# Kernel optimization log

Measured on AMD Instinct MI355X. Metric: run time of the kernel, lower is better.

The kernel has to match this reference:

```python
import jax, jax.numpy as jnp
import numpy as np

B, S, D = 2, 2048, 2048
H, HD = 16, 128
F = 8192
LC = 512
EPS = 1e-6


def _linear_params(k, din, dout):
    k1, k2 = jax.random.split(k)
    w = jax.random.normal(k1, (din, dout), jnp.float32) * 0.02
    b = jax.random.normal(k2, (dout,), jnp.float32) * 0.02
    return w, b


def setup_inputs() -> dict:
    key = jax.random.key(0)
    ks = jax.random.split(key, 20)
    inp = {}
    inp["x"] = jax.random.normal(ks[0], (B, S, D), jnp.float32)
    inp["e"] = jax.random.normal(ks[1], (B, 6, D), jnp.float32) * 0.1
    inp["context"] = jax.random.normal(ks[2], (B, LC, D), jnp.float32)
    # per-token rotary angles [S, HD//2] (Wan builds such a table from 3D grid)
    inp["freqs"] = jax.random.uniform(ks[3], (S, HD // 2), jnp.float32) * (2.0 * np.pi)
    inp["modulation"] = jax.random.normal(ks[4], (1, 6, D), jnp.float32) / np.sqrt(D)
    names = ["sq", "sk", "sv", "so", "cq", "ck", "cv", "co"]
    for i, nm in enumerate(names):
        w, b = _linear_params(ks[5 + i], D, D)
        inp[nm + "_w"], inp[nm + "_b"] = w, b
    inp["f1_w"], inp["f1_b"] = _linear_params(ks[13], D, F)
    inp["f2_w"], inp["f2_b"] = _linear_params(ks[14], F, D)
    inp["snq"] = jnp.ones((D,), jnp.float32)
    inp["snk"] = jnp.ones((D,), jnp.float32)
    inp["cnq"] = jnp.ones((D,), jnp.float32)
    inp["cnk"] = jnp.ones((D,), jnp.float32)
    return inp


def _rmsnorm(x, w):
    # WanRMSNorm: x * rsqrt(mean(x^2) + eps) * weight
    return x * jax.lax.rsqrt(jnp.mean(x * x, axis=-1, keepdims=True) + EPS) * w


def _layernorm(x):
    # elementwise_affine=False LayerNorm
    m = jnp.mean(x, axis=-1, keepdims=True)
    v = jnp.mean((x - m) ** 2, axis=-1, keepdims=True)
    return (x - m) * jax.lax.rsqrt(v + EPS)


def _rope(x, ang):
    # x: [B, S, H, HD]; ang: [S, HD//2]; adjacent pairs rotated (view_as_complex)
    c = jnp.cos(ang)[None, :, None, :]
    s = jnp.sin(ang)[None, :, None, :]
    xr, xi = x[..., 0::2], x[..., 1::2]
    out = jnp.stack([xr * c - xi * s, xr * s + xi * c], axis=-1)
    return out.reshape(x.shape)


def _attn(q, k, v):
    # q: [B,Sq,H,HD], k/v: [B,Sk,H,HD] -> [B,Sq,H,HD]
    scores = jnp.einsum("bqhd,bkhd->bhqk", q, k) / np.sqrt(HD)
    probs = jax.nn.softmax(scores, axis=-1)
    return jnp.einsum("bhqk,bkhd->bqhd", probs, v)


def reference(x, e, context, freqs, modulation,
              sq_w, sq_b, sk_w, sk_b, sv_w, sv_b, so_w, so_b, snq, snk,
              cq_w, cq_b, ck_w, ck_b, cv_w, cv_b, co_w, co_b, cnq, cnk,
              f1_w, f1_b, f2_w, f2_b):
    em = modulation + e  # [B,6,D]
    e0, e1, e2, e3, e4, e5 = [em[:, i:i + 1, :] for i in range(6)]

    # self-attention with AdaLN modulation
    tx = _layernorm(x) * (1.0 + e1) + e0
    q = _rmsnorm(tx @ sq_w + sq_b, snq).reshape(B, S, H, HD)
    k = _rmsnorm(tx @ sk_w + sk_b, snk).reshape(B, S, H, HD)
    v = (tx @ sv_w + sv_b).reshape(B, S, H, HD)
    q, k = _rope(q, freqs), _rope(k, freqs)
    y = _attn(q, k, v).reshape(B, S, D) @ so_w + so_b
    x = x + y * e2

    # cross-attention (norm3 = Identity since cross_attn_norm=False)
    q = _rmsnorm(x @ cq_w + cq_b, cnq).reshape(B, S, H, HD)
    k = _rmsnorm(context @ ck_w + ck_b, cnk).reshape(B, LC, H, HD)
    v = (context @ cv_w + cv_b).reshape(B, LC, H, HD)
    x = x + (_attn(q, k, v).reshape(B, S, D) @ co_w + co_b)

    # FFN with AdaLN modulation
    tx = _layernorm(x) * (1.0 + e4) + e3
    y = jax.nn.gelu(tx @ f1_w + f1_b, approximate=True) @ f2_w + f2_b
    x = x + y * e5
    return x
```

## Files before the change

### kernel.cpp

```cpp
#include <hip/hip_runtime.h>
#include <hip/hip_bf16.h>

using bf16 = __hip_bfloat16;
typedef __attribute__((ext_vector_type(8))) short bf16x8;
typedef __attribute__((ext_vector_type(4))) float f32x4;
typedef const __attribute__((address_space(1))) unsigned int* gp_t;
typedef __attribute__((address_space(3))) unsigned int* sp_t;

#define B_   2
#define S_   2048
#define D_   2048
#define H_   16
#define HD_  128
#define F_   8192
#define LC_  512
#define ESTRIDE (6*D_)

__device__ __forceinline__ float bsum4(float v, float* rs) {
  #pragma unroll
  for (int o = 32; o; o >>= 1) v += __shfl_down(v, o, 64);
  int lane = threadIdx.x & 63, w = threadIdx.x >> 6;
  if (!lane) rs[w] = v;
  __syncthreads();
  float r = rs[0] + rs[1] + rs[2] + rs[3];
  __syncthreads();
  return r;
}
__device__ __forceinline__ float bmax4(float v, float* rs) {
  #pragma unroll
  for (int o = 32; o; o >>= 1) v = fmaxf(v, __shfl_down(v, o, 64));
  int lane = threadIdx.x & 63, w = threadIdx.x >> 6;
  if (!lane) rs[w] = v;
  __syncthreads();
  float r = fmaxf(fmaxf(rs[0], rs[1]), fmaxf(rs[2], rs[3]));
  __syncthreads();
  return r;
}

__global__ void k_addmod(const float* __restrict__ e, const float* __restrict__ mod,
                         float* __restrict__ em) {
  int i = blockIdx.x * 256 + threadIdx.x;
  em[i] = e[i] + mod[i % (6 * D_)];
}

__global__ void k_f2b(const float* __restrict__ in, bf16* __restrict__ out) {
  int i = blockIdx.x * 256 + threadIdx.x;
  out[i] = __float2bfloat16(in[i]);
}

__global__ void k_copy_f32(const float* __restrict__ in, float* __restrict__ out) {
  int i = blockIdx.x * 256 + threadIdx.x;
  out[i] = in[i];
}

__global__ void k_tr_f2b(const float* __restrict__ in, bf16* __restrict__ out,
                         int K, int N) {
  __shared__ float tile[64][65];
  int kb = blockIdx.y << 6, nb = blockIdx.x << 6;
  int x = threadIdx.x & 63, y = threadIdx.x >> 6;
  #pragma unroll
  for (int r = y; r < 64; r += 4) tile[r][x] = in[(size_t)(kb + r) * N + nb + x];
  __syncthreads();
  #pragma unroll
  for (int r = y; r < 64; r += 4)
    out[(size_t)(nb + r) * K + kb + x] = __float2bfloat16(tile[x][r]);
}

__global__ void k_tr_b2b(const bf16* __restrict__ in, bf16* __restrict__ out,
                         int R, int C, long long sIn, long long sOut) {
  in  += (long long)blockIdx.z * sIn;
  out += (long long)blockIdx.z * sOut;
  __shared__ bf16 tile[64][65];
  int rb = blockIdx.y << 6, cb = blockIdx.x << 6;
  int x = threadIdx.x & 63, y = threadIdx.x >> 6;
  #pragma unroll
  for (int r = y; r < 64; r += 4) tile[r][x] = in[(size_t)(rb + r) * C + cb + x];
  __syncthreads();
  #pragma unroll
  for (int r = y; r < 64; r += 4) out[(size_t)(cb + r) * R + rb + x] = tile[x][r];
}

__global__ void k_ln_mod(const float* __restrict__ x, const float* __restrict__ em,
                         int i0, int i1, bf16* __restrict__ out, int s_per_b) {
  __shared__ float rs[4];
  int row = blockIdx.x, t = threadIdx.x;
  int b = row / s_per_b;
  const float* xr = x + (size_t)row * D_;
  float vals[8], s = 0.f, ss = 0.f;
  #pragma unroll
  for (int j = 0; j < 8; j++) {
    float v = xr[t + j * 256];
    vals[j] = v; s += v; ss += v * v;
  }
  s  = bsum4(s, rs);
  ss = bsum4(ss, rs);
  float mean = s * (1.f / D_);
  float var  = ss * (1.f / D_) - mean * mean;
  float inv  = rsqrtf(var + 1e-6f);
  const float* e0 = em + ((size_t)b * 6 + i0) * D_;
  const float* e1 = em + ((size_t)b * 6 + i1) * D_;
  bf16* orow = out + (size_t)row * D_;
  #pragma unroll
  for (int j = 0; j < 8; j++) {
    int c = t + j * 256;
    orow[c] = __float2bfloat16((vals[j] - mean) * inv * (1.f + e1[c]) + e0[c]);
  }
}

__global__ void k_rms_rope(bf16* __restrict__ buf, const float* __restrict__ w,
                           const float* __restrict__ freqs, int do_rope, int s_per_b) {
  __shared__ float rs[4];
  int row = blockIdx.x, t = threadIdx.x;
  bf16* pr = buf + (size_t)row * D_;
  float4 raw = *(const float4*)(pr + (size_t)t * 8);
  bf16* hb = (bf16*)&raw;
  float v[8], ss = 0.f;
  #pragma unroll
  for (int j = 0; j < 8; j++) { v[j] = __bfloat162float(hb[j]); ss += v[j] * v[j]; }
  ss = bsum4(ss, rs);
  float inv = rsqrtf(ss * (1.f / D_) + 1e-6f);
  int base = t * 8;
  #pragma unroll
  for (int j = 0; j < 8; j++) v[j] = v[j] * inv * w[base + j];
  if (do_rope) {
    int s = row % s_per_b;
    const float* fr = freqs + (size_t)s * (HD_ / 2) + ((base & (HD_ - 1)) >> 1);
    #pragma unroll
    for (int p = 0; p < 4; p++) {
      float ang = fr[p];
      float c = cosf(ang), sn = sinf(ang);
      float xr = v[2 * p], xi = v[2 * p + 1];
      v[2 * p]     = xr * c - xi * sn;
      v[2 * p + 1] = xr * sn + xi * c;
    }
  }
  float4 ow; bf16* ho = (bf16*)&ow;
  #pragma unroll
  for (int j = 0; j < 8; j++) ho[j] = __float2bfloat16(v[j]);
  *(float4*)(pr + (size_t)t * 8) = ow;
}

template <int EPT>
__global__ void k_softmax(bf16* __restrict__ buf, int N) {
  __shared__ float rs[4];
  int row = blockIdx.x, t = threadIdx.x;
  bf16* pr = buf + (size_t)row * N;
  float v[EPT], mx = -1e30f;
  #pragma unroll
  for (int j = 0; j < EPT; j++) { v[j] = __bfloat162float(pr[t + j * 256]); mx = fmaxf(mx, v[j]); }
  mx = bmax4(mx, rs);
  float s = 0.f;
  #pragma unroll
  for (int j = 0; j < EPT; j++) { v[j] = __expf(v[j] - mx); s += v[j]; }
  s = bsum4(s, rs);
  float invs = 1.f / s;
  #pragma unroll
  for (int j = 0; j < EPT; j++) pr[t + j * 256] = __float2bfloat16(v[j] * invs);
}

__device__ __forceinline__ void xcd_swizzle(int& bx, int& by) {
  int nx = gridDim.x, ny = gridDim.y;
  if ((nx & 7) == 0) {
    int flat = by * nx + bx;
    int xcd = flat & 7;
    int idx = flat >> 3;
    int sx = nx >> 3;
    bx = xcd * sx + (idx % sx);
    by = idx / sx;
    (void)ny;
  }
}

template <int EPI>
__global__ __launch_bounds__(256) void gemm_bt(
    const bf16* __restrict__ A, int lda, long long sA,
    const bf16* __restrict__ Bt, int ldb, long long sB,
    const float* __restrict__ bias,
    bf16* __restrict__ Cb, int ldc, long long sCb,
    float* __restrict__ Cf, const float* __restrict__ Xin,
    float scale, const float* __restrict__ evec, int s_per_b,
    int K) {
  __shared__ __align__(16) bf16 As[128][32];
  __shared__ __align__(16) bf16 Bs[128][32];
  const int z = blockIdx.z;
  A  += (long long)z * sA;
  Bt += (long long)z * sB;
  int bx = blockIdx.x, by = blockIdx.y;
  xcd_swizzle(bx, by);
  const int m0 = by * 128, n0 = bx * 128;
  const int t = threadIdx.x;
  const int w = t >> 6, lane = t & 63;
  const int wrow = (w >> 1) * 64, wcol = (w & 1) * 64;
  const int quad = lane >> 4, l16 = lane & 15;

  f32x4 zero = {0.f, 0.f, 0.f, 0.f};
  f32x4 acc[4][4];
  #pragma unroll
  for (int i = 0; i < 4; i++)
    #pragma unroll
    for (int j = 0; j < 4; j++) acc[i][j] = zero;

  for (int k0 = 0; k0 < K; k0 += 32) {
    #pragma unroll
    for (int i = 0; i < 2; i++) {
      int c = t + i * 256;
      int r = c >> 2, col = (c & 3) * 8;
      __builtin_amdgcn_global_load_lds(
          (gp_t)(A + (size_t)(m0 + r) * lda + k0 + col),
          (sp_t)(&As[0][0] + (size_t)(w * 64 + i * 256) * 8), 16, 0, 0);
      __builtin_amdgcn_global_load_lds(
          (gp_t)(Bt + (size_t)(n0 + r) * ldb + k0 + col),
          (sp_t)(&Bs[0][0] + (size_t)(w * 64 + i * 256) * 8), 16, 0, 0);
    }
    __syncthreads();
    bf16x8 af[4], bfr[4];
    #pragma unroll
    for (int mi = 0; mi < 4; mi++) af[mi]  = *(const bf16x8*)(&As[wrow + mi * 16 + l16][quad * 8]);
    #pragma unroll
    for (int ni = 0; ni < 4; ni++) bfr[ni] = *(const bf16x8*)(&Bs[wcol + ni * 16 + l16][quad * 8]);
    #pragma unroll
    for (int mi = 0; mi < 4; mi++)
      #pragma unroll
      for (int ni = 0; ni < 4; ni++)
        acc[mi][ni] = __builtin_amdgcn_mfma_f32_16x16x32_bf16(af[mi], bfr[ni], acc[mi][ni], 0, 0, 0);
    __syncthreads();
  }

  #pragma unroll
  for (int mi = 0; mi < 4; mi++) {
    #pragma unroll
    for (int r = 0; r < 4; r++) {
      int gm = m0 + wrow + mi * 16 + quad * 4 + r;
      #pragma unroll
      for (int ni = 0; ni < 4; ni++) {
        int gn = n0 + wcol + ni * 16 + l16;
        float v = acc[mi][ni][r];
        if (EPI == 0) {
          if (bias) v += bias[gn];
          Cb[(long long)z * sCb + (size_t)gm * ldc + gn] = __float2bfloat16(v);
        } else if (EPI == 1) {
          Cb[(long long)z * sCb + (size_t)gm * ldc + gn] = __float2bfloat16(v * scale);
        } else if (EPI == 3) {
          v += bias[gn];
          float g = 0.5f * v * (1.f + tanhf(0.7978845608028654f * (v + 0.044715f * v * v * v)));
          Cb[(long long)z * sCb + (size_t)gm * ldc + gn] = __float2bfloat16(g);
        } else {
          v += bias[gn];
          if (evec) v *= evec[(size_t)(gm / s_per_b) * ESTRIDE + gn];
          float o = Xin[(size_t)gm * ldc + gn] + v;
          Cf[(size_t)gm * ldc + gn] = o;
          if (Cb) Cb[(size_t)gm * ldc + gn] = __float2bfloat16(o);
        }
      }
    }
  }
}

__global__ __launch_bounds__(256) void gemm64(
    const bf16* __restrict__ A, int lda, long long sA,
    const bf16* __restrict__ Bt, int ldb, long long sB,
    bf16* __restrict__ Cb, int ldc, long long sCb,
    int K) {
  __shared__ __align__(16) bf16 As[64][32];
  __shared__ __align__(16) bf16 Bs[64][32];
  const int z = blockIdx.z;
  A  += (long long)z * sA;
  Bt += (long long)z * sB;
  const int m0 = blockIdx.y * 64, n0 = blockIdx.x * 64;
  const int t = threadIdx.x;
  const int w = t >> 6, lane = t & 63;
  const int wrow = (w >> 1) * 32, wcol = (w & 1) * 32;
  const int quad = lane >> 4, l16 = lane & 15;

  f32x4 zero = {0.f, 0.f, 0.f, 0.f};
  f32x4 acc[2][2];
  #pragma unroll
  for (int i = 0; i < 2; i++)
    #pragma unroll
    for (int j = 0; j < 2; j++) acc[i][j] = zero;

  for (int k0 = 0; k0 < K; k0 += 32) {
    {
      int r = t >> 2, col = (t & 3) * 8;
      __builtin_amdgcn_global_load_lds(
          (gp_t)(A + (size_t)(m0 + r) * lda + k0 + col),
          (sp_t)(&As[0][0] + (size_t)(w * 64) * 8), 16, 0, 0);
      __builtin_amdgcn_global_load_lds(
          (gp_t)(Bt + (size_t)(n0 + r) * ldb + k0 + col),
          (sp_t)(&Bs[0][0] + (size_t)(w * 64) * 8), 16, 0, 0);
    }
    __syncthreads();
    bf16x8 af[2], bfr[2];
    #pragma unroll
    for (int mi = 0; mi < 2; mi++) af[mi]  = *(const bf16x8*)(&As[wrow + mi * 16 + l16][quad * 8]);
    #pragma unroll
    for (int ni = 0; ni < 2; ni++) bfr[ni] = *(const bf16x8*)(&Bs[wcol + ni * 16 + l16][quad * 8]);
    #pragma unroll
    for (int mi = 0; mi < 2; mi++)
      #pragma unroll
      for (int ni = 0; ni < 2; ni++)
        acc[mi][ni] = __builtin_amdgcn_mfma_f32_16x16x32_bf16(af[mi], bfr[ni], acc[mi][ni], 0, 0, 0);
    __syncthreads();
  }

  #pragma unroll
  for (int mi = 0; mi < 2; mi++) {
    #pragma unroll
    for (int r = 0; r < 4; r++) {
      int gm = m0 + wrow + mi * 16 + quad * 4 + r;
      #pragma unroll
      for (int ni = 0; ni < 2; ni++) {
        int gn = n0 + wcol + ni * 16 + l16;
        Cb[(long long)z * sCb + (size_t)gm * ldc + gn] = __float2bfloat16(acc[mi][ni][r]);
      }
    }
  }
}

extern "C" void kernel_launch(void* const* d_in, const int* in_sizes, int n_in,
                              void* d_out, int out_size, void* d_ws, size_t ws_size,
                              hipStream_t stream) {
  const float* x     = (const float*)d_in[0];
  const float* e     = (const float*)d_in[1];
  const float* ctx   = (const float*)d_in[2];
  const float* freqs = (const float*)d_in[3];
  const float* modu  = (const float*)d_in[4];
  const float* sq_w = (const float*)d_in[5];  const float* sq_b = (const float*)d_in[6];
  const float* sk_w = (const float*)d_in[7];  const float* sk_b = (const float*)d_in[8];
  const float* sv_w = (const float*)d_in[9];  const float* sv_b = (const float*)d_in[10];
  const float* so_w = (const float*)d_in[11]; const float* so_b = (const float*)d_in[12];
  const float* cq_w = (const float*)d_in[13]; const float* cq_b = (const float*)d_in[14];
  const float* ck_w = (const float*)d_in[15]; const float* ck_b = (const float*)d_in[16];
  const float* cv_w = (const float*)d_in[17]; const float* cv_b = (const float*)d_in[18];
  const float* co_w = (const float*)d_in[19]; const float* co_b = (const float*)d_in[20];
  const float* f1_w = (const float*)d_in[21]; const float* f1_b = (const float*)d_in[22];
  const float* f2_w = (const float*)d_in[23]; const float* f2_b = (const float*)d_in[24];
  const float* snq  = (const float*)d_in[25]; const float* snk  = (const float*)d_in[26];
  const float* cnq  = (const float*)d_in[27]; const float* cnk  = (const float*)d_in[28];
  float* out = (float*)d_out;

  const size_t MD = (size_t)B_ * S_ * D_;

  char* W = (char*)d_ws;
  size_t off = 0;
  auto alloc = [&](size_t bytes) -> char* {
    char* p = W + off; off += (bytes + 255) & ~(size_t)255; return p;
  };
  float* em  = (float*)alloc((size_t)B_ * 6 * D_ * 4);
  bf16* wT   = (bf16*)alloc((size_t)F_ * D_ * 2);
  bf16* vb   = (bf16*)alloc(MD * 2);
  bf16* tx   = (bf16*)alloc(MD * 2);
  bf16* qb   = (bf16*)alloc(MD * 2);
  bf16* kb   = (bf16*)alloc(MD * 2);
  bf16* vt   = (bf16*)alloc(MD * 2);
  bf16* attnout = (bf16*)alloc(MD * 2);
  bf16* ctxb = (bf16*)alloc((size_t)B_ * LC_ * D_ * 2);
  bf16* kc   = (bf16*)alloc((size_t)B_ * LC_ * D_ * 2);
  bf16* vc   = (bf16*)alloc((size_t)B_ * LC_ * D_ * 2);
  bf16* vtc  = (bf16*)alloc((size_t)B_ * LC_ * D_ * 2);
  bf16* scores8 = wT;
  bf16* scoresC = wT;
  bf16* mid = qb;
  if (off > ws_size) {
    k_copy_f32<<<(int)(MD / 256), 256, 0, stream>>>(x, out);
    return;
  }

  const float qk_scale = 0.08838834764831845f;

  k_addmod<<<(B_ * 6 * D_) / 256, 256, 0, stream>>>(e, modu, em);
  k_f2b<<<(B_ * LC_ * D_) / 256, 256, 0, stream>>>(ctx, ctxb);

  k_ln_mod<<<B_ * S_, 256, 0, stream>>>(x, em, 0, 1, tx, S_);
  k_tr_f2b<<<dim3(D_ / 64, D_ / 64), 256, 0, stream>>>(sq_w, wT, D_, D_);
  gemm_bt<0><<<dim3(16, 32, 1), 256, 0, stream>>>(tx, D_, 0, wT, D_, 0, sq_b,
      qb, D_, 0, nullptr, nullptr, 1.f, nullptr, S_, D_);
  k_tr_f2b<<<dim3(D_ / 64, D_ / 64), 256, 0, stream>>>(sk_w, wT, D_, D_);
  gemm_bt<0><<<dim3(16, 32, 1), 256, 0, stream>>>(tx, D_, 0, wT, D_, 0, sk_b,
      kb, D_, 0, nullptr, nullptr, 1.f, nullptr, S_, D_);
  k_tr_f2b<<<dim3(D_ / 64, D_ / 64), 256, 0, stream>>>(sv_w, wT, D_, D_);
  gemm_bt<0><<<dim3(16, 32, 1), 256, 0, stream>>>(tx, D_, 0, wT, D_, 0, sv_b,
      vb, D_, 0, nullptr, nullptr, 1.f, nullptr, S_, D_);
  k_rms_rope<<<B_ * S_, 256, 0, stream>>>(qb, snq, freqs, 1, S_);
  k_rms_rope<<<B_ * S_, 256, 0, stream>>>(kb, snk, freqs, 1, S_);
  k_tr_b2b<<<dim3(D_ / 64, S_ / 64, B_), 256, 0, stream>>>(vb, vt, S_, D_,
      (long long)S_ * D_, (long long)D_ * S_);

  for (int b = 0; b < B_; b++) {
    for (int hc = 0; hc < 2; hc++) {
      const int h0 = hc * 8;
      const bf16* Aq = qb + (size_t)b * S_ * D_ + h0 * HD_;
      const bf16* Bk = kb + (size_t)b * S_ * D_ + h0 * HD_;
      gemm_bt<1><<<dim3(16, 16, 8), 256, 0, stream>>>(Aq, D_, HD_, Bk, D_, HD_, nullptr,
          scores8, S_, (long long)S_ * S_, nullptr, nullptr, qk_scale, nullptr, S_, HD_);
      k_softmax<8><<<8 * S_, 256, 0, stream>>>(scores8, S_);
      const bf16* Bv = vt + ((size_t)b * D_ + h0 * HD_) * S_;
      gemm64<<<dim3(2, 32, 8), 256, 0, stream>>>(scores8, S_, (long long)S_ * S_,
          Bv, S_, (long long)HD_ * S_,
          attnout + (size_t)b * S_ * D_ + h0 * HD_, D_, HD_, S_);
    }
  }
  k_tr_f2b<<<dim3(D_ / 64, D_ / 64), 256, 0, stream>>>(so_w, wT, D_, D_);
  gemm_bt<2><<<dim3(16, 32, 1), 256, 0, stream>>>(attnout, D_, 0, wT, D_, 0, so_b,
      tx, D_, 0, out, x, 1.f, em + 2 * D_, S_, D_);

  k_tr_f2b<<<dim3(D_ / 64, D_ / 64), 256, 0, stream>>>(cq_w, wT, D_, D_);
  gemm_bt<0><<<dim3(16, 32, 1), 256, 0, stream>>>(tx, D_, 0, wT, D_, 0, cq_b,
      qb, D_, 0, nullptr, nullptr, 1.f, nullptr, S_, D_);
  k_rms_rope<<<B_ * S_, 256, 0, stream>>>(qb, cnq, nullptr, 0, S_);
  k_tr_f2b<<<dim3(D_ / 64, D_ / 64), 256, 0, stream>>>(ck_w, wT, D_, D_);
  gemm_bt<0><<<dim3(16, 8, 1), 256, 0, stream>>>(ctxb, D_, 0, wT, D_, 0, ck_b,
      kc, D_, 0, nullptr, nullptr, 1.f, nullptr, S_, D_);
  k_rms_rope<<<B_ * LC_, 256, 0, stream>>>(kc, cnk, nullptr, 0, S_);
  k_tr_f2b<<<dim3(D_ / 64, D_ / 64), 256, 0, stream>>>(cv_w, wT, D_, D_);
  gemm_bt<0><<<dim3(16, 8, 1), 256, 0, stream>>>(ctxb, D_, 0, wT, D_, 0, cv_b,
      vc, D_, 0, nullptr, nullptr, 1.f, nullptr, S_, D_);
  k_tr_b2b<<<dim3(D_ / 64, LC_ / 64, B_), 256, 0, stream>>>(vc, vtc, LC_, D_,
      (long long)LC_ * D_, (long long)D_ * LC_);

  for (int b = 0; b < B_; b++) {
    gemm_bt<1><<<dim3(4, 16, 16), 256, 0, stream>>>(qb + (size_t)b * S_ * D_, D_, HD_,
        kc + (size_t)b * LC_ * D_, D_, HD_, nullptr,
        scoresC, LC_, (long long)S_ * LC_, nullptr, nullptr, qk_scale, nullptr, S_, HD_);
    k_softmax<2><<<16 * S_, 256, 0, stream>>>(scoresC, LC_);
    gemm64<<<dim3(2, 32, 16), 256, 0, stream>>>(scoresC, LC_, (long long)S_ * LC_,
        vtc + (size_t)b * D_ * LC_, LC_, (long long)HD_ * LC_,
        attnout + (size_t)b * S_ * D_, D_, HD_, LC_);
  }
  k_tr_f2b<<<dim3(D_ / 64, D_ / 64), 256, 0, stream>>>(co_w, wT, D_, D_);
  gemm_bt<2><<<dim3(16, 32, 1), 256, 0, stream>>>(attnout, D_, 0, wT, D_, 0, co_b,
      nullptr, D_, 0, out, out, 1.f, nullptr, S_, D_);

  k_ln_mod<<<B_ * S_, 256, 0, stream>>>(out, em, 3, 4, tx, S_);
  k_tr_f2b<<<dim3(F_ / 64, D_ / 64), 256, 0, stream>>>(f1_w, wT, D_, F_);
  gemm_bt<3><<<dim3(64, 32, 1), 256, 0, stream>>>(tx, D_, 0, wT, D_, 0, f1_b,
      mid, F_, 0, nullptr, nullptr, 1.f, nullptr, S_, D_);
  k_tr_f2b<<<dim3(D_ / 64, F_ / 64), 256, 0, stream>>>(f2_w, wT, F_, D_);
  gemm_bt<2><<<dim3(16, 32, 1), 256, 0, stream>>>(mid, F_, 0, wT, F_, 0, f2_b,
      nullptr, D_, 0, out, out, 1.f, em + 5 * D_, S_, F_);
}
```

Before: 1.848 ms.

## Fuse Q/K projections, vectorize transposes and softmax, reuse 128-tile GEMM for PV

Concatenates the Q and K weights and biases so both self-attention projections run as one wider GEMM writing an interleaved QK buffer. Transposes now use two-element vector stores, and softmax loads and stores contiguous vectors per thread. The separate 64-tile PV kernel is removed in favour of the 128-tile GEMM. GELU tanh is rewritten as an equivalent sigmoid form using __expf. The PV GEMM now launches far fewer blocks (1x16x8), which may cut occupancy.

```diff
diff --git a/kernel.cpp b/kernel.cpp
--- a/kernel.cpp
+++ b/kernel.cpp
@@ -16,6 +16,13 @@
 #define LC_  512
 #define ESTRIDE (6*D_)
 
+__device__ __forceinline__ unsigned short bu(bf16 h) {
+  return __builtin_bit_cast(unsigned short, h);
+}
+__device__ __forceinline__ unsigned short f2bu(float f) {
+  return __builtin_bit_cast(unsigned short, __float2bfloat16(f));
+}
+
 __device__ __forceinline__ float bsum4(float v, float* rs) {
   #pragma unroll
   for (int o = 32; o; o >>= 1) v += __shfl_down(v, o, 64);
@@ -51,6 +58,12 @@
 __global__ void k_copy_f32(const float* __restrict__ in, float* __restrict__ out) {
   int i = blockIdx.x * 256 + threadIdx.x;
   out[i] = in[i];
+}
+
+__global__ void k_cat2(const float* __restrict__ a, const float* __restrict__ b,
+                       float* __restrict__ o) {
+  int i = blockIdx.x * 256 + threadIdx.x;
+  o[i] = (i < D_) ? a[i] : b[i - D_];
 }
 
 __global__ void k_tr_f2b(const float* __restrict__ in, bf16* __restrict__ out,
@@ -61,23 +74,34 @@
   #pragma unroll
   for (int r = y; r < 64; r += 4) tile[r][x] = in[(size_t)(kb + r) * N + nb + x];
   __syncthreads();
-  #pragma unroll
-  for (int r = y; r < 64; r += 4)
-    out[(size_t)(nb + r) * K + kb + x] = __float2bfloat16(tile[x][r]);
+  int lx = threadIdx.x & 31, sy = threadIdx.x >> 5;
+  #pragma unroll
+  for (int r = sy; r < 64; r += 8) {
+    ushort2 v;
+    v.x = f2bu(tile[2 * lx][r]);
+    v.y = f2bu(tile[2 * lx + 1][r]);
+    *(ushort2*)&out[(size_t)(nb + r) * K + kb + 2 * lx] = v;
+  }
 }
 
 __global__ void k_tr_b2b(const bf16* __restrict__ in, bf16* __restrict__ out,
-                         int R, int C, long long sIn, long long sOut) {
+                         int R, int C, int ldin, long long sIn, long long sOut) {
   in  += (long long)blockIdx.z * sIn;
   out += (long long)blockIdx.z * sOut;
-  __shared__ bf16 tile[64][65];
+  __shared__ bf16 tile[64][66];
   int rb = blockIdx.y << 6, cb = blockIdx.x << 6;
-  int x = threadIdx.x & 63, y = threadIdx.x >> 6;
-  #pragma unroll
-  for (int r = y; r < 64; r += 4) tile[r][x] = in[(size_t)(rb + r) * C + cb + x];
-  __syncthreads();
-  #pragma unroll
-  for (int r = y; r < 64; r += 4) out[(size_t)(cb + r) * R + rb + x] = tile[x][r];
+  int lx = threadIdx.x & 31, sy = threadIdx.x >> 5;
+  #pragma unroll
+  for (int r = sy; r < 64; r += 8)
+    *(uint*)&tile[r][2 * lx] = *(const uint*)&in[(size_t)(rb + r) * ldin + cb + 2 * lx];
+  __syncthreads();
+  #pragma unroll
+  for (int c = sy; c < 64; c += 8) {
+    ushort2 v;
+    v.x = bu(tile[2 * lx][c]);
+    v.y = bu(tile[2 * lx + 1][c]);
+    *(ushort2*)&out[(size_t)(cb + c) * R + rb + 2 * lx] = v;
+  }
 }
 
 __global__ void k_ln_mod(const float* __restrict__ x, const float* __restrict__ em,
@@ -107,11 +131,11 @@
   }
 }
 
-__global__ void k_rms_rope(bf16* __restrict__ buf, const float* __restrict__ w,
+__global__ void k_rms_rope(bf16* __restrict__ buf, int ld, const float* __restrict__ w,
                            const float* __restrict__ freqs, int do_rope, int s_per_b) {
   __shared__ float rs[4];
   int row = blockIdx.x, t = threadIdx.x;
-  bf16* pr = buf + (size_t)row * D_;
+  bf16* pr = buf + (size_t)row * ld;
   float4 raw = *(const float4*)(pr + (size_t)t * 8);
   bf16* hb = (bf16*)&raw;
   float v[8], ss = 0.f;
@@ -144,10 +168,13 @@
 __global__ void k_softmax(bf16* __restrict__ buf, int N) {
   __shared__ float rs[4];
   int row = blockIdx.x, t = threadIdx.x;
-  bf16* pr = buf + (size_t)row * N;
+  bf16* pr = buf + (size_t)row * N + (size_t)t * EPT;
+  bf16 h[EPT];
+  if constexpr (EPT == 8) { *(float4*)h = *(const float4*)pr; }
+  else                    { *(uint*)h   = *(const uint*)pr; }
   float v[EPT], mx = -1e30f;
   #pragma unroll
-  for (int j = 0; j < EPT; j++) { v[j] = __bfloat162float(pr[t + j * 256]); mx = fmaxf(mx, v[j]); }
+  for (int j = 0; j < EPT; j++) { v[j] = __bfloat162float(h[j]); mx = fmaxf(mx, v[j]); }
   mx = bmax4(mx, rs);
   float s = 0.f;
   #pragma unroll
@@ -155,20 +182,9 @@
   s = bsum4(s, rs);
   float invs = 1.f / s;
   #pragma unroll
-  for (int j = 0; j < EPT; j++) pr[t + j * 256] = __float2bfloat16(v[j] * invs);
-}
-
-__device__ __forceinline__ void xcd_swizzle(int& bx, int& by) {
-  int nx = gridDim.x, ny = gridDim.y;
-  if ((nx & 7) == 0) {
-    int flat = by * nx + bx;
-    int xcd = flat & 7;
-    int idx = flat >> 3;
-    int sx = nx >> 3;
-    bx = xcd * sx + (idx % sx);
-    by = idx / sx;
-    (void)ny;
-  }
+  for (int j = 0; j < EPT; j++) h[j] = __float2bfloat16(v[j] * invs);
+  if constexpr (EPT == 8) { *(float4*)pr = *(float4*)h; }
+  else                    { *(uint*)pr   = *(uint*)h; }
 }
 
 template <int EPI>
@@ -186,7 +202,15 @@
   A  += (long long)z * sA;
   Bt += (long long)z * sB;
   int bx = blockIdx.x, by = blockIdx.y;
-  xcd_swizzle(bx, by);
+  {
+    int nx = gridDim.x;
+    if ((nx & 7) == 0) {
+      int flat = by * nx + bx;
+      int xcd = flat & 7, idx = flat >> 3, sx = nx >> 3;
+      bx = xcd * sx + (idx % sx);
+      by = idx / sx;
+    }
+  }
   const int m0 = by * 128, n0 = bx * 128;
   const int t = threadIdx.x;
   const int w = t >> 6, lane = t & 63;
@@ -242,7 +266,8 @@
           Cb[(long long)z * sCb + (size_t)gm * ldc + gn] = __float2bfloat16(v * scale);
         } else if (EPI == 3) {
           v += bias[gn];
-          float g = 0.5f * v * (1.f + tanhf(0.7978845608028654f * (v + 0.044715f * v * v * v)));
+          float u = 1.5957691216057308f * (v + 0.044715f * v * v * v);
+          float g = v / (1.f + __expf(-u));
           Cb[(long long)z * sCb + (size_t)gm * ldc + gn] = __float2bfloat16(g);
         } else {
           v += bias[gn];
@@ -251,67 +276,6 @@
           Cf[(size_t)gm * ldc + gn] = o;
           if (Cb) Cb[(size_t)gm * ldc + gn] = __float2bfloat16(o);
         }
-      }
-    }
-  }
-}
-
-__global__ __launch_bounds__(256) void gemm64(
-    const bf16* __restrict__ A, int lda, long long sA,
-    const bf16* __restrict__ Bt, int ldb, long long sB,
-    bf16* __restrict__ Cb, int ldc, long long sCb,
-    int K) {
-  __shared__ __align__(16) bf16 As[64][32];
-  __shared__ __align__(16) bf16 Bs[64][32];
-  const int z = blockIdx.z;
-  A  += (long long)z * sA;
-  Bt += (long long)z * sB;
-  const int m0 = blockIdx.y * 64, n0 = blockIdx.x * 64;
-  const int t = threadIdx.x;
-  const int w = t >> 6, lane = t & 63;
-  const int wrow = (w >> 1) * 32, wcol = (w & 1) * 32;
-  const int quad = lane >> 4, l16 = lane & 15;
-
-  f32x4 zero = {0.f, 0.f, 0.f, 0.f};
-  f32x4 acc[2][2];
-  #pragma unroll
-  for (int i = 0; i < 2; i++)
-    #pragma unroll
-    for (int j = 0; j < 2; j++) acc[i][j] = zero;
-
-  for (int k0 = 0; k0 < K; k0 += 32) {
-    {
-      int r = t >> 2, col = (t & 3) * 8;
-      __builtin_amdgcn_global_load_lds(
-          (gp_t)(A + (size_t)(m0 + r) * lda + k0 + col),
-          (sp_t)(&As[0][0] + (size_t)(w * 64) * 8), 16, 0, 0);
-      __builtin_amdgcn_global_load_lds(
-          (gp_t)(Bt + (size_t)(n0 + r) * ldb + k0 + col),
-          (sp_t)(&Bs[0][0] + (size_t)(w * 64) * 8), 16, 0, 0);
-    }
-    __syncthreads();
-    bf16x8 af[2], bfr[2];
-    #pragma unroll
-    for (int mi = 0; mi < 2; mi++) af[mi]  = *(const bf16x8*)(&As[wrow + mi * 16 + l16][quad * 8]);
-    #pragma unroll
-    for (int ni = 0; ni < 2; ni++) bfr[ni] = *(const bf16x8*)(&Bs[wcol + ni * 16 + l16][quad * 8]);
-    #pragma unroll
-    for (int mi = 0; mi < 2; mi++)
-      #pragma unroll
-      for (int ni = 0; ni < 2; ni++)
-        acc[mi][ni] = __builtin_amdgcn_mfma_f32_16x16x32_bf16(af[mi], bfr[ni], acc[mi][ni], 0, 0, 0);
-    __syncthreads();
-  }
-
-  #pragma unroll
-  for (int mi = 0; mi < 2; mi++) {
-    #pragma unroll
-    for (int r = 0; r < 4; r++) {
-      int gm = m0 + wrow + mi * 16 + quad * 4 + r;
-      #pragma unroll
-      for (int ni = 0; ni < 2; ni++) {
-        int gn = n0 + wcol + ni * 16 + l16;
-        Cb[(long long)z * sCb + (size_t)gm * ldc + gn] = __float2bfloat16(acc[mi][ni][r]);
       }
     }
   }
@@ -348,19 +312,21 @@
   };
   float* em  = (float*)alloc((size_t)B_ * 6 * D_ * 4);
   bf16* wT   = (bf16*)alloc((size_t)F_ * D_ * 2);
+  bf16* tx   = (bf16*)alloc(MD * 2);
   bf16* vb   = (bf16*)alloc(MD * 2);
-  bf16* tx   = (bf16*)alloc(MD * 2);
-  bf16* qb   = (bf16*)alloc(MD * 2);
-  bf16* kb   = (bf16*)alloc(MD * 2);
+  bf16* qk   = (bf16*)alloc((size_t)B_ * S_ * 2 * D_ * 2);
   bf16* vt   = (bf16*)alloc(MD * 2);
   bf16* attnout = (bf16*)alloc(MD * 2);
   bf16* ctxb = (bf16*)alloc((size_t)B_ * LC_ * D_ * 2);
   bf16* kc   = (bf16*)alloc((size_t)B_ * LC_ * D_ * 2);
   bf16* vc   = (bf16*)alloc((size_t)B_ * LC_ * D_ * 2);
   bf16* vtc  = (bf16*)alloc((size_t)B_ * LC_ * D_ * 2);
+  float* bqk = (float*)alloc((size_t)2 * D_ * 4);
   bf16* scores8 = wT;
   bf16* scoresC = wT;
-  bf16* mid = qb;
+  bf16* qb2 = vb;
+  bf16* mid = qk;
+  bf16* wTv = wT + (size_t)2 * D_ * D_;
   if (off > ws_size) {
     k_copy_f32<<<(int)(MD / 256), 256, 0, stream>>>(x, out);
     return;
@@ -370,34 +336,35 @@
 
   k_addmod<<<(B_ * 6 * D_) / 256, 256, 0, stream>>>(e, modu, em);
   k_f2b<<<(B_ * LC_ * D_) / 256, 256, 0, stream>>>(ctx, ctxb);
+  k_cat2<<<(2 * D_) / 256, 256, 0, stream>>>(sq_b, sk_b, bqk);
 
   k_ln_mod<<<B_ * S_, 256, 0, stream>>>(x, em, 0, 1, tx, S_);
   k_tr_f2b<<<dim3(D_ / 64, D_ / 64), 256, 0, stream>>>(sq_w, wT, D_, D_);
-  gemm_bt<0><<<dim3(16, 32, 1), 256, 0, stream>>>(tx, D_, 0, wT, D_, 0, sq_b,
-      qb, D_, 0, nullptr, nullptr, 1.f, nullptr, S_, D_);
-  k_tr_f2b<<<dim3(D_ / 64, D_ / 64), 256, 0, stream>>>(sk_w, wT, D_, D_);
-  gemm_bt<0><<<dim3(16, 32, 1), 256, 0, stream>>>(tx, D_, 0, wT, D_, 0, sk_b,
-      kb, D_, 0, nullptr, nullptr, 1.f, nullptr, S_, D_);
-  k_tr_f2b<<<dim3(D_ / 64, D_ / 64), 256, 0, stream>>>(sv_w, wT, D_, D_);
-  gemm_bt<0><<<dim3(16, 32, 1), 256, 0, stream>>>(tx, D_, 0, wT, D_, 0, sv_b,
+  k_tr_f2b<<<dim3(D_ / 64, D_ / 64), 256, 0, stream>>>(sk_w, wT + (size_t)D_ * D_, D_, D_);
+  k_tr_f2b<<<dim3(D_ / 64, D_ / 64), 256, 0, stream>>>(sv_w, wTv, D_, D_);
+  gemm_bt<0><<<dim3(32, 32, 1), 256, 0, stream>>>(tx, D_, 0, wT, D_, 0, bqk,
+      qk, 2 * D_, 0, nullptr, nullptr, 1.f, nullptr, S_, D_);
+  gemm_bt<0><<<dim3(16, 32, 1), 256, 0, stream>>>(tx, D_, 0, wTv, D_, 0, sv_b,
       vb, D_, 0, nullptr, nullptr, 1.f, nullptr, S_, D_);
-  k_rms_rope<<<B_ * S_, 256, 0, stream>>>(qb, snq, freqs, 1, S_);
-  k_rms_rope<<<B_ * S_, 256, 0, stream>>>(kb, snk, freqs, 1, S_);
-  k_tr_b2b<<<dim3(D_ / 64, S_ / 64, B_), 256, 0, stream>>>(vb, vt, S_, D_,
+  k_rms_rope<<<B_ * S_, 256, 0, stream>>>(qk, 2 * D_, snq, freqs, 1, S_);
+  k_rms_rope<<<B_ * S_, 256, 0, stream>>>(qk + D_, 2 * D_, snk, freqs, 1, S_);
+  k_tr_b2b<<<dim3(D_ / 64, S_ / 64, B_), 256, 0, stream>>>(vb, vt, S_, D_, D_,
       (long long)S_ * D_, (long long)D_ * S_);
 
   for (int b = 0; b < B_; b++) {
     for (int hc = 0; hc < 2; hc++) {
       const int h0 = hc * 8;
-      const bf16* Aq = qb + (size_t)b * S_ * D_ + h0 * HD_;
-      const bf16* Bk = kb + (size_t)b * S_ * D_ + h0 * HD_;
-      gemm_bt<1><<<dim3(16, 16, 8), 256, 0, stream>>>(Aq, D_, HD_, Bk, D_, HD_, nullptr,
-          scores8, S_, (long long)S_ * S_, nullptr, nullptr, qk_scale, nullptr, S_, HD_);
+      const bf16* Aq = qk + (size_t)b * S_ * 2 * D_ + h0 * HD_;
+      const bf16* Bk = qk + (size_t)b * S_ * 2 * D_ + D_ + h0 * HD_;
+      gemm_bt<1><<<dim3(16, 16, 8), 256, 0, stream>>>(Aq, 2 * D_, HD_, Bk, 2 * D_, HD_,
+          nullptr, scores8, S_, (long long)S_ * S_, nullptr, nullptr, qk_scale,
+          nullptr, S_, HD_);
       k_softmax<8><<<8 * S_, 256, 0, stream>>>(scores8, S_);
       const bf16* Bv = vt + ((size_t)b * D_ + h0 * HD_) * S_;
-      gemm64<<<dim3(2, 32, 8), 256, 0, stream>>>(scores8, S_, (long long)S_ * S_,
-          Bv, S_, (long long)HD_ * S_,
-          attnout + (size_t)b * S_ * D_ + h0 * HD_, D_, HD_, S_);
+      gemm_bt<0><<<dim3(1, 16, 8), 256, 0, stream>>>(scores8, S_, (long long)S_ * S_,
+          Bv, S_, (long long)HD_ * S_, nullptr,
+          attnout + (size_t)b * S_ * D_ + h0 * HD_, D_, HD_,
+          nullptr, nullptr, 1.f, nullptr, S_, S_);
     }
   }
   k_tr_f2b<<<dim3(D_ / 64, D_ / 64), 256, 0, stream>>>(so_w, wT, D_, D_);
@@ -406,26 +373,27 @@
 
   k_tr_f2b<<<dim3(D_ / 64, D_ / 64), 256, 0, stream>>>(cq_w, wT, D_, D_);
   gemm_bt<0><<<dim3(16, 32, 1), 256, 0, stream>>>(tx, D_, 0, wT, D_, 0, cq_b,
-      qb, D_, 0, nullptr, nullptr, 1.f, nullptr, S_, D_);
-  k_rms_rope<<<B_ * S_, 256, 0, stream>>>(qb, cnq, nullptr, 0, S_);
+      qb2, D_, 0, nullptr, nullptr, 1.f, nullptr, S_, D_);
+  k_rms_rope<<<B_ * S_, 256, 0, stream>>>(qb2, D_, cnq, nullptr, 0, S_);
   k_tr_f2b<<<dim3(D_ / 64, D_ / 64), 256, 0, stream>>>(ck_w, wT, D_, D_);
   gemm_bt<0><<<dim3(16, 8, 1), 256, 0, stream>>>(ctxb, D_, 0, wT, D_, 0, ck_b,
       kc, D_, 0, nullptr, nullptr, 1.f, nullptr, S_, D_);
-  k_rms_rope<<<B_ * LC_, 256, 0, stream>>>(kc, cnk, nullptr, 0, S_);
+  k_rms_rope<<<B_ * LC_, 256, 0, stream>>>(kc, D_, cnk, nullptr, 0, S_);
   k_tr_f2b<<<dim3(D_ / 64, D_ / 64), 256, 0, stream>>>(cv_w, wT, D_, D_);
   gemm_bt<0><<<dim3(16, 8, 1), 256, 0, stream>>>(ctxb, D_, 0, wT, D_, 0, cv_b,
       vc, D_, 0, nullptr, nullptr, 1.f, nullptr, S_, D_);
-  k_tr_b2b<<<dim3(D_ / 64, LC_ / 64, B_), 256, 0, stream>>>(vc, vtc, LC_, D_,
+  k_tr_b2b<<<dim3(D_ / 64, LC_ / 64, B_), 256, 0, stream>>>(vc, vtc, LC_, D_, D_,
       (long long)LC_ * D_, (long long)D_ * LC_);
 
   for (int b = 0; b < B_; b++) {
-    gemm_bt<1><<<dim3(4, 16, 16), 256, 0, stream>>>(qb + (size_t)b * S_ * D_, D_, HD_,
+    gemm_bt<1><<<dim3(4, 16, 16), 256, 0, stream>>>(qb2 + (size_t)b * S_ * D_, D_, HD_,
         kc + (size_t)b * LC_ * D_, D_, HD_, nullptr,
         scoresC, LC_, (long long)S_ * LC_, nullptr, nullptr, qk_scale, nullptr, S_, HD_);
     k_softmax<2><<<16 * S_, 256, 0, stream>>>(scoresC, LC_);
-    gemm64<<<dim3(2, 32, 16), 256, 0, stream>>>(scoresC, LC_, (long long)S_ * LC_,
-        vtc + (size_t)b * D_ * LC_, LC_, (long long)HD_ * LC_,
-        attnout + (size_t)b * S_ * D_, D_, HD_, LC_);
+    gemm_bt<0><<<dim3(1, 16, 16), 256, 0, stream>>>(scoresC, LC_, (long long)S_ * LC_,
+        vtc + (size_t)b * D_ * LC_, LC_, (long long)HD_ * LC_, nullptr,
+        attnout + (size_t)b * S_ * D_, D_, HD_,
+        nullptr, nullptr, 1.f, nullptr, S_, LC_);
   }
   k_tr_f2b<<<dim3(D_ / 64, D_ / 64), 256, 0, stream>>>(co_w, wT, D_, D_);
   gemm_bt<2><<<dim3(16, 32, 1), 256, 0, stream>>>(attnout, D_, 0, wT, D_, 0, co_b,
```

Result: slower. 1.935 ms (+4.7%).
